# Optimization experiments

Hardware: AMD Instinct MI355X
Metric: run time of the kernel (lower is better)

## Reference

```python
import jax, jax.numpy as jnp
import numpy as np
from jax import lax


def setup_inputs() -> dict:
    key = jax.random.key(0)
    k1, k2, k3, k4 = jax.random.split(key, 4)
    H = 2048
    L = 3
    hidden_states = jax.random.normal(k1, (2, 4096, H), dtype=jnp.float32)
    Win = jax.random.normal(k2, (3 * H, H), dtype=jnp.float32) * (H ** -0.5)
    conv_w = jax.random.normal(k3, (H, 1, L), dtype=jnp.float32) * (L ** -0.5)
    Wout = jax.random.normal(k4, (H, H), dtype=jnp.float32) * (H ** -0.5)
    return {"hidden_states": hidden_states, "Win": Win, "conv_w": conv_w, "Wout": Wout}


def reference(hidden_states, Win, conv_w, Wout):
    H = hidden_states.shape[-1]
    L = conv_w.shape[-1]
    BCx = jnp.einsum('bsh,oh->bso', hidden_states, Win)  # (b, s, 3H)
    B, C, x = jnp.split(BCx, 3, axis=-1)
    Bx = jnp.transpose(B * x, (0, 2, 1))  # (b, H, s)
    # depthwise causal conv: left-pad L-1 so output length == s (torch pads both
    # sides then slices [..., :seqlen]; left-only padding is equivalent)
    conv_out = lax.conv_general_dilated(
        Bx, conv_w, window_strides=(1,), padding=[(L - 1, 0)],
        feature_group_count=H, dimension_numbers=('NCH', 'OIH', 'NCH'))
    y = C * jnp.transpose(conv_out, (0, 2, 1))  # (b, s, H)
    return jnp.einsum('bsh,oh->bso', y, Wout)
```

## Files before the change

kernel.cpp:

```cpp
#include <hip/hip_runtime.h>
#include <hip/hip_bf16.h>

typedef unsigned short u16;
typedef __attribute__((ext_vector_type(8))) short bf16x8;
typedef __attribute__((ext_vector_type(4))) float f32x4;

static __device__ __forceinline__ u16 f2bf(float f) {
    unsigned u = __float_as_uint(f);
    unsigned r = (u + 0x7fffu + ((u >> 16) & 1u)) >> 16;
    return (u16)r;
}
static __device__ __forceinline__ float bf2f(u16 u) {
    return __uint_as_float(((unsigned)u) << 16);
}

static __device__ __forceinline__ void async_copy16(const void* gptr, void* lptr) {
    __builtin_amdgcn_global_load_lds(
        (const __attribute__((address_space(1))) void*)gptr,
        (__attribute__((address_space(3))) void*)lptr, 16, 0, 0);
}

__global__ __launch_bounds__(256)
void cvt_all(const float* __restrict__ a, const float* __restrict__ b,
             const float* __restrict__ c,
             u16* __restrict__ oa, u16* __restrict__ ob, u16* __restrict__ oc) {
#pragma unroll
    for (int it = 0; it < 8; it++) {
        long li = ((long)it << 20) + (long)blockIdx.x * 256 + threadIdx.x;
        const float* src; u16* dst; long u;
        if (li < 4194304)      { src = a; dst = oa; u = li; }
        else if (li < 7340032) { src = b; dst = ob; u = li - 4194304; }
        else                   { src = c; dst = oc; u = li - 7340032; }
        long i = u * 4;
        float4 f = *(const float4*)(src + i);
        u16 o[4] = { f2bf(f.x), f2bf(f.y), f2bf(f.z), f2bf(f.w) };
        *(uint2*)(dst + i) = *(const uint2*)o;
    }
}

template<bool FUSED>
__global__ __launch_bounds__(512, 2)
void gemm_bt8(const u16* __restrict__ A, const u16* __restrict__ B,
              u16* __restrict__ oBx, u16* __restrict__ oC,
              float* __restrict__ oF, int M, int N, int K) {
    __shared__ __align__(16) u16 lds[65536];

    const int t    = threadIdx.x;
    const int lane = t & 63;
    const int wm   = (t >> 6) >> 2;
    const int wn   = (t >> 6) & 3;
    const int l15  = lane & 15;
    const int hi   = lane >> 4;
    const int l7   = lane & 7;

    const int id   = blockIdx.y * gridDim.x + blockIdx.x;
    const int cpx  = gridDim.x >> 3;
    const int bx   = (id & 7) * cpx + ((id >> 3) % cpx);
    const int by   = (id >> 3) / cpx;
    const long rowA = (long)by * 256;

    const int pl0 = t >> 3;
    const int slotcol = ((t & 7) ^ (pl0 & 7)) * 8;
    const u16* Asrc[2][2]; const u16* Bsrc[2][2];
#pragma unroll
    for (int h = 0; h < 2; h++) {
        int gA0 = h * 64 + pl0;
        int gA1 = 128 + h * 64 + pl0;
        Asrc[h][0] = A + (rowA + gA0) * (long)K + slotcol;
        Asrc[h][1] = A + (rowA + gA1) * (long)K + slotcol;
    }
    if (FUSED && bx < 16) {
        const long rB = (long)bx * 128 + pl0;
        Bsrc[0][0] = B + rB * (long)K + slotcol;
        Bsrc[0][1] = Bsrc[0][0] + 64 * (long)K;
        Bsrc[1][0] = B + (4096 + rB) * (long)K + slotcol;
        Bsrc[1][1] = Bsrc[1][0] + 64 * (long)K;
    } else {
        const long rowB = FUSED ? (2048 + (long)(bx - 16) * 256)
                                : (long)bx * 256;
#pragma unroll
        for (int h = 0; h < 2; h++) {
            int nB0 = (pl0 >> 5) * 64 + h * 32 + (pl0 & 31);
            Bsrc[h][0] = B + (rowB + nB0) * (long)K + slotcol;
            Bsrc[h][1] = Bsrc[h][0] + 128 * (long)K;
        }
    }
    const int t8 = t * 8;

    auto STAGE_A = [&](int bufo, int h, int kk) {
        u16* d = lds + bufo + h * 8192 + t8;
        async_copy16(Asrc[h][0] + kk, d);
        async_copy16(Asrc[h][1] + kk, d + 4096);
    };
    auto STAGE_B = [&](int bufo, int h, int kk) {
        u16* d = lds + bufo + 16384 + h * 8192 + t8;
        async_copy16(Bsrc[h][0] + kk, d);
        async_copy16(Bsrc[h][1] + kk, d + 4096);
    };

    const int aBase = wm * 4096 + l15 * 64;
    const int bBase = 16384 + wn * 2048 + l15 * 64;
    const int sOff0 = (hi ^ l7) * 8;
    const int sOff1 = ((4 + hi) ^ l7) * 8;

    bf16x8 af[4][2], ba[2][2], bb[2][2];
    f32x4 acc[8][4] = {};

    auto LOAD_A2 = [&](int bufo, int Mq, int mb) {
        const u16* p = lds + bufo + Mq * 8192 + aBase + mb * 1024;
        af[mb][0]     = *(const bf16x8*)(p + sOff0);
        af[mb][1]     = *(const bf16x8*)(p + sOff1);
        af[mb + 1][0] = *(const bf16x8*)(p + 1024 + sOff0);
        af[mb + 1][1] = *(const bf16x8*)(p + 1024 + sOff1);
    };
    auto LOAD_B = [&](bf16x8 (&bg)[2][2], int bufo, int Nq) {
        const u16* p = lds + bufo + Nq * 8192 + bBase;
        bg[0][0] = *(const bf16x8*)(p + sOff0);
        bg[0][1] = *(const bf16x8*)(p + sOff1);
        bg[1][0] = *(const bf16x8*)(p + 1024 + sOff0);
        bg[1][1] = *(const bf16x8*)(p + 1024 + sOff1);
    };
    auto MFMA_H = [&](int Mq, int Nq, int mb, bf16x8 (&bg)[2][2]) {
        __builtin_amdgcn_s_setprio(1);
#pragma unroll
        for (int ks = 0; ks < 2; ks++)
#pragma unroll
            for (int m = mb; m < mb + 2; m++)
#pragma unroll
                for (int n = 0; n < 2; n++)
                    acc[Mq * 4 + m][Nq * 2 + n] =
                        __builtin_amdgcn_mfma_f32_16x16x32_bf16(
                            af[m][ks], bg[n][ks], acc[Mq * 4 + m][Nq * 2 + n],
                            0, 0, 0);
        __builtin_amdgcn_s_setprio(0);
    };

#define BAR()   __builtin_amdgcn_s_barrier()
#define SB()    __builtin_amdgcn_sched_barrier(0)
#define LGKM(n) do { asm volatile("s_waitcnt lgkmcnt(" #n ")" ::: "memory"); \
                     __builtin_amdgcn_sched_barrier(0); } while (0)
#define VM(n)   asm volatile("s_waitcnt vmcnt(" #n ")" ::: "memory")

#define TILE(BC, BN, KK)                                                     \
                                                              \
    LOAD_B(ba, BC, 0); LOAD_A2(BC, 0, 0); SB(); LOAD_A2(BC, 0, 2);           \
    STAGE_A(BN, 0, KK); VM(2);                                               \
    LGKM(4); MFMA_H(0, 0, 0, ba); LGKM(0); MFMA_H(0, 0, 2, ba); BAR();       \
                                                              \
    LOAD_B(bb, BC, 1);                                                       \
    STAGE_B(BN, 0, KK);                                                      \
    LGKM(0); MFMA_H(0, 1, 0, bb); MFMA_H(0, 1, 2, bb); BAR();                \
                                                              \
    LOAD_A2(BC, 1, 0); SB(); LOAD_A2(BC, 1, 2);                              \
    STAGE_A(BN, 1, KK);                                                      \
    LGKM(4); MFMA_H(1, 1, 0, bb); LGKM(0); MFMA_H(1, 1, 2, bb); BAR();       \
                                                              \
    STAGE_B(BN, 1, KK); VM(4);                                               \
    MFMA_H(1, 0, 0, ba); MFMA_H(1, 0, 2, ba); BAR();

    STAGE_A(0, 0, 0);  STAGE_B(0, 0, 0);
    STAGE_A(0, 1, 0);  STAGE_B(0, 1, 0);
    asm volatile("s_waitcnt vmcnt(0)" ::: "memory");
    BAR();

    const int NT = K >> 6;
#pragma unroll 1
    for (int i = 0; i < NT; i += 2) {
        int k1 = (i + 1) << 6;
        int k2 = (i + 2 < NT) ? (i + 2) << 6 : k1;
        TILE(0, 32768, k1);
        TILE(32768, 0, k2);
    }
    asm volatile("s_waitcnt vmcnt(0) lgkmcnt(0)" ::: "memory");

#undef TILE
#undef VM
#undef LGKM
#undef SB
#undef BAR

    const long rBase = rowA + wm * 128 + hi * 4;
    if (FUSED && bx < 16) {
        const long hBase = (long)bx * 128 + wn * 32 + l15;
#pragma unroll
        for (int mi = 0; mi < 8; mi++) {
#pragma unroll
            for (int n = 0; n < 2; n++) {
                long col = hBase + n * 16;
#pragma unroll
                for (int r = 0; r < 4; r++) {
                    long row = rBase + mi * 16 + r;
                    float v = acc[mi][n][r] * acc[mi][n + 2][r];
                    oBx[row * 2048 + col] = f2bf(v);
                }
            }
        }
    } else if (FUSED) {
        const long colBase = (long)(bx - 16) * 256 + wn * 64 + l15;
#pragma unroll
        for (int mi = 0; mi < 8; mi++)
#pragma unroll
            for (int nj = 0; nj < 4; nj++)
#pragma unroll
                for (int r = 0; r < 4; r++) {
                    long row = rBase + mi * 16 + r;
                    oC[row * 2048 + colBase + nj * 16] = f2bf(acc[mi][nj][r]);
                }
    } else {
        const long colBase = (long)bx * 256 + wn * 64 + l15;
#pragma unroll
        for (int mi = 0; mi < 8; mi++)
#pragma unroll
            for (int nj = 0; nj < 4; nj++)
#pragma unroll
                for (int r = 0; r < 4; r++) {
                    long row = rBase + mi * 16 + r;
                    oF[row * (long)N + colBase + nj * 16] = acc[mi][nj][r];
                }
    }
}

union U16x8 { uint4 v; u16 u[8]; };

__global__ __launch_bounds__(256)
void conv_fuse(const u16* __restrict__ Bx, const u16* __restrict__ Cc,
               const float* __restrict__ cw, u16* __restrict__ y) {
    const int r0 = blockIdx.x * 8;
    const int h0 = threadIdx.x * 8;
    const int batch = r0 >> 12;

    U16x8 P[10];
#pragma unroll
    for (int ii = 0; ii < 10; ii++) {
        int g = r0 - 2 + ii;
        if (g >= 0 && (g >> 12) == batch)
            P[ii].v = *(const uint4*)(Bx + (long)g * 2048 + h0);
        else
            P[ii].v = make_uint4(0, 0, 0, 0);
    }
    float bx[10][8];
#pragma unroll
    for (int ii = 0; ii < 10; ii++)
#pragma unroll
        for (int i = 0; i < 8; i++)
            bx[ii][i] = bf2f(P[ii].u[i]);

    float w0[8], w1[8], w2[8];
#pragma unroll
    for (int i = 0; i < 8; i++) {
        int h = h0 + i;
        w0[i] = cw[h * 3];
        w1[i] = cw[h * 3 + 1];
        w2[i] = cw[h * 3 + 2];
    }

#pragma unroll
    for (int jj = 0; jj < 8; jj++) {
        U16x8 Cv, o;
        Cv.v = *(const uint4*)(Cc + (long)(r0 + jj) * 2048 + h0);
#pragma unroll
        for (int i = 0; i < 8; i++) {
            float v = w2[i] * bx[jj + 2][i] + w1[i] * bx[jj + 1][i]
                    + w0[i] * bx[jj][i];
            o.u[i] = f2bf(v * bf2f(Cv.u[i]));
        }
        *(uint4*)(y + (long)(r0 + jj) * 2048 + h0) = o.v;
    }
}

extern "C" void kernel_launch(void* const* d_in, const int* in_sizes, int n_in,
                              void* d_out, int out_size, void* d_ws, size_t ws_size,
                              hipStream_t stream) {
    const float* hs   = (const float*)d_in[0];
    const float* Win  = (const float*)d_in[1];
    const float* cw   = (const float*)d_in[2];
    const float* Wout = (const float*)d_in[3];
    float* out = (float*)d_out;

    char* ws = (char*)d_ws;
    u16* hsb   = (u16*)(ws);
    u16* Winb  = (u16*)(ws +  33554432);
    u16* Woutb = (u16*)(ws +  58720256);
    u16* bxb   = (u16*)(ws +  67108864);
    u16* cb    = (u16*)(ws + 100663296);
    u16* yb    = (u16*)(ws + 134217728);

    cvt_all<<<4096, 256, 0, stream>>>(hs, Win, Wout, hsb, Winb, Woutb);

    gemm_bt8<true ><<<dim3(24, 32), 512, 0, stream>>>(
        hsb, Winb, bxb, cb, nullptr, 8192, 2048, 2048);

    conv_fuse<<<1024, 256, 0, stream>>>(bxb, cb, cw, yb);

    gemm_bt8<false><<<dim3(8, 32), 512, 0, stream>>>(
        yb, Woutb, nullptr, nullptr, out, 8192, 2048, 2048);
}
```

Baseline: 413.2 us.

## Switch GEMM inner product from 16x16x32 to 32x32x16 bf16 MFMA tiles

```diff
diff --git a/kernel.cpp b/kernel.cpp
--- a/kernel.cpp
+++ b/kernel.cpp
@@ -3,7 +3,7 @@
 
 typedef unsigned short u16;
 typedef __attribute__((ext_vector_type(8))) short bf16x8;
-typedef __attribute__((ext_vector_type(4))) float f32x4;
+typedef __attribute__((ext_vector_type(16))) float f32x16;
 
 static __device__ __forceinline__ u16 f2bf(float f) {
     unsigned u = __float_as_uint(f);
@@ -49,8 +49,8 @@
     const int lane = t & 63;
     const int wm   = (t >> 6) >> 2;
     const int wn   = (t >> 6) & 3;
-    const int l15  = lane & 15;
-    const int hi   = lane >> 4;
+    const int l32  = lane & 31;
+    const int hi1  = lane >> 5;
     const int l7   = lane & 7;
 
     const int id   = blockIdx.y * gridDim.x + blockIdx.x;
@@ -98,42 +98,35 @@
         async_copy16(Bsrc[h][1] + kk, d + 4096);
     };
 
-    const int aBase = wm * 4096 + l15 * 64;
-    const int bBase = 16384 + wn * 2048 + l15 * 64;
-    const int sOff0 = (hi ^ l7) * 8;
-    const int sOff1 = ((4 + hi) ^ l7) * 8;
-
-    bf16x8 af[4][2], ba[2][2], bb[2][2];
-    f32x4 acc[8][4] = {};
-
-    auto LOAD_A2 = [&](int bufo, int Mq, int mb) {
-        const u16* p = lds + bufo + Mq * 8192 + aBase + mb * 1024;
-        af[mb][0]     = *(const bf16x8*)(p + sOff0);
-        af[mb][1]     = *(const bf16x8*)(p + sOff1);
-        af[mb + 1][0] = *(const bf16x8*)(p + 1024 + sOff0);
-        af[mb + 1][1] = *(const bf16x8*)(p + 1024 + sOff1);
-    };
-    auto LOAD_B = [&](bf16x8 (&bg)[2][2], int bufo, int Nq) {
+    const int aBase = (wm * 64 + l32) * 64;
+    const int bBase = 16384 + (wn * 32 + l32) * 64;
+    const int cof[4] = { ((0 * 2 + hi1) ^ l7) * 8, ((1 * 2 + hi1) ^ l7) * 8,
+                         ((2 * 2 + hi1) ^ l7) * 8, ((3 * 2 + hi1) ^ l7) * 8 };
+
+    bf16x8 af[2][4], ba[4], bb[4];
+    f32x16 acc[4][2] = {};
+
+    auto LOAD_A = [&](int bufo, int Mq, int m) {
+        const u16* p = lds + bufo + Mq * 8192 + aBase + m * 2048;
+#pragma unroll
+        for (int mf = 0; mf < 4; mf++)
+            af[m][mf] = *(const bf16x8*)(p + cof[mf]);
+    };
+    auto LOAD_B = [&](bf16x8 (&bg)[4], int bufo, int Nq) {
         const u16* p = lds + bufo + Nq * 8192 + bBase;
-        bg[0][0] = *(const bf16x8*)(p + sOff0);
-        bg[0][1] = *(const bf16x8*)(p + sOff1);
-        bg[1][0] = *(const bf16x8*)(p + 1024 + sOff0);
-        bg[1][1] = *(const bf16x8*)(p + 1024 + sOff1);
-    };
-    auto MFMA_H = [&](int Mq, int Nq, int mb, bf16x8 (&bg)[2][2]) {
-        __builtin_amdgcn_s_setprio(1);
-#pragma unroll
-        for (int ks = 0; ks < 2; ks++)
-#pragma unroll
-            for (int m = mb; m < mb + 2; m++)
-#pragma unroll
-                for (int n = 0; n < 2; n++)
-                    acc[Mq * 4 + m][Nq * 2 + n] =
-                        __builtin_amdgcn_mfma_f32_16x16x32_bf16(
-                            af[m][ks], bg[n][ks], acc[Mq * 4 + m][Nq * 2 + n],
-                            0, 0, 0);
-        __builtin_amdgcn_s_setprio(0);
-    };
+#pragma unroll
+        for (int mf = 0; mf < 4; mf++)
+            bg[mf] = *(const bf16x8*)(p + cof[mf]);
+    };
+
+#define MF4(MQ, NQ, m, BG) do {                                              \
+    __builtin_amdgcn_s_setprio(1);                                           \
+    _Pragma("unroll")                                                        \
+    for (int mf = 0; mf < 4; mf++)                                           \
+        acc[(MQ) * 2 + (m)][NQ] = __builtin_amdgcn_mfma_f32_32x32x16_bf16(   \
+            af[m][mf], BG[mf], acc[(MQ) * 2 + (m)][NQ], 0, 0, 0);            \
+    __builtin_amdgcn_s_setprio(0);                                           \
+} while (0)
 
 #define BAR()   __builtin_amdgcn_s_barrier()
 #define SB()    __builtin_amdgcn_sched_barrier(0)
@@ -143,20 +136,20 @@
 
 #define TILE(BC, BN, KK)                                                     \
                                                               \
-    LOAD_B(ba, BC, 0); LOAD_A2(BC, 0, 0); SB(); LOAD_A2(BC, 0, 2);           \
+    LOAD_B(ba, BC, 0); LOAD_A(BC, 0, 0); SB(); LOAD_A(BC, 0, 1);             \
     STAGE_A(BN, 0, KK); VM(2);                                               \
-    LGKM(4); MFMA_H(0, 0, 0, ba); LGKM(0); MFMA_H(0, 0, 2, ba); BAR();       \
+    LGKM(4); MF4(0, 0, 0, ba); LGKM(0); MF4(0, 0, 1, ba); BAR();             \
                                                               \
     LOAD_B(bb, BC, 1);                                                       \
     STAGE_B(BN, 0, KK);                                                      \
-    LGKM(0); MFMA_H(0, 1, 0, bb); MFMA_H(0, 1, 2, bb); BAR();                \
-                                                              \
-    LOAD_A2(BC, 1, 0); SB(); LOAD_A2(BC, 1, 2);                              \
+    LGKM(0); MF4(0, 1, 0, bb); MF4(0, 1, 1, bb); BAR();                      \
+                                                              \
+    LOAD_A(BC, 1, 0); SB(); LOAD_A(BC, 1, 1);                                \
     STAGE_A(BN, 1, KK);                                                      \
-    LGKM(4); MFMA_H(1, 1, 0, bb); LGKM(0); MFMA_H(1, 1, 2, bb); BAR();       \
+    LGKM(4); MF4(1, 1, 0, bb); LGKM(0); MF4(1, 1, 1, bb); BAR();             \
                                                               \
     STAGE_B(BN, 1, KK); VM(4);                                               \
-    MFMA_H(1, 0, 0, ba); MFMA_H(1, 0, 2, ba); BAR();
+    MF4(1, 0, 0, ba); MF4(1, 0, 1, ba); BAR();
 
     STAGE_A(0, 0, 0);  STAGE_B(0, 0, 0);
     STAGE_A(0, 1, 0);  STAGE_B(0, 1, 0);
@@ -177,46 +170,47 @@
 #undef VM
 #undef LGKM
 #undef SB
+#undef MF4
 #undef BAR
 
-    const long rBase = rowA + wm * 128 + hi * 4;
     if (FUSED && bx < 16) {
-        const long hBase = (long)bx * 128 + wn * 32 + l15;
-#pragma unroll
-        for (int mi = 0; mi < 8; mi++) {
-#pragma unroll
-            for (int n = 0; n < 2; n++) {
-                long col = hBase + n * 16;
-#pragma unroll
-                for (int r = 0; r < 4; r++) {
-                    long row = rBase + mi * 16 + r;
-                    float v = acc[mi][n][r] * acc[mi][n + 2][r];
-                    oBx[row * 2048 + col] = f2bf(v);
+        const long hCol = (long)bx * 128 + wn * 32 + l32;
+#pragma unroll
+        for (int i = 0; i < 4; i++) {
+            long rB = rowA + wm * 128 + (i >> 1) * 64 + (i & 1) * 32;
+#pragma unroll
+            for (int r = 0; r < 16; r++) {
+                long row = rB + (r & 3) + 8 * (r >> 2) + 4 * hi1;
+                float v = acc[i][0][r] * acc[i][1][r];
+                oBx[row * 2048 + hCol] = f2bf(v);
+            }
+        }
+    } else if (FUSED) {
+        const long colB = (long)(bx - 16) * 256 + wn * 64 + l32;
+#pragma unroll
+        for (int i = 0; i < 4; i++) {
+            long rB = rowA + wm * 128 + (i >> 1) * 64 + (i & 1) * 32;
+#pragma unroll
+            for (int nq = 0; nq < 2; nq++)
+#pragma unroll
+                for (int r = 0; r < 16; r++) {
+                    long row = rB + (r & 3) + 8 * (r >> 2) + 4 * hi1;
+                    oC[row * 2048 + colB + nq * 32] = f2bf(acc[i][nq][r]);
                 }
-            }
-        }
-    } else if (FUSED) {
-        const long colBase = (long)(bx - 16) * 256 + wn * 64 + l15;
-#pragma unroll
-        for (int mi = 0; mi < 8; mi++)
-#pragma unroll
-            for (int nj = 0; nj < 4; nj++)
-#pragma unroll
-                for (int r = 0; r < 4; r++) {
-                    long row = rBase + mi * 16 + r;
-                    oC[row * 2048 + colBase + nj * 16] = f2bf(acc[mi][nj][r]);
+        }
+    } else {
+        const long colB = (long)bx * 256 + wn * 64 + l32;
+#pragma unroll
+        for (int i = 0; i < 4; i++) {
+            long rB = rowA + wm * 128 + (i >> 1) * 64 + (i & 1) * 32;
+#pragma unroll
+            for (int nq = 0; nq < 2; nq++)
+#pragma unroll
+                for (int r = 0; r < 16; r++) {
+                    long row = rB + (r & 3) + 8 * (r >> 2) + 4 * hi1;
+                    oF[row * (long)N + colB + nq * 32] = acc[i][nq][r];
                 }
-    } else {
-        const long colBase = (long)bx * 256 + wn * 64 + l15;
-#pragma unroll
-        for (int mi = 0; mi < 8; mi++)
-#pragma unroll
-            for (int nj = 0; nj < 4; nj++)
-#pragma unroll
-                for (int r = 0; r < 4; r++) {
-                    long row = rBase + mi * 16 + r;
-                    oF[row * (long)N + colBase + nj * 16] = acc[mi][nj][r];
-                }
+        }
     }
 }
 
```

Result: slower. 447.2 us (+8.2%).
